# Optimization experiments

Hardware: AMD Instinct MI355X
Metric: run time of the kernel (lower is better)

The kernel has to match this reference:

```python
import jax, jax.numpy as jnp
import numpy as np


def setup_inputs() -> dict:
    key = jax.random.key(0)
    k1, k2 = jax.random.split(key)
    x = jax.random.normal(k1, (64, 64, 64, 64), dtype=jnp.float32)
    embeddings = jax.random.normal(k2, (400, 64), dtype=jnp.float32) * 0.1
    return {"x": x, "embeddings": embeddings}


def reference(x, embeddings):
    D = embeddings.shape[1]
    flat_x = x.reshape(-1, D)  # [N, D]
    # squared L2 distance via sum-of-squares + matmul: [N, K]
    distances = (
        jnp.sum(flat_x * flat_x, axis=1, keepdims=True)
        + jnp.sum(embeddings * embeddings, axis=1)
        - 2.0 * jnp.matmul(flat_x, embeddings.T)
    )
    encoding_indices = jnp.argmin(distances, axis=1)  # [N]
    quantized = jnp.take(embeddings, encoding_indices, axis=0)  # [N, D]
    return quantized.reshape(x.shape)
```

## Files before the change

kernel.cpp:

```cpp
#include <hip/hip_runtime.h>
#include <hip/hip_bf16.h>

#define D 64
#define K 400
#define KT 25
#define BLOCK 512
#define WPB (BLOCK / 64)
#define MA 4

typedef _Float16 f16x8 __attribute__((ext_vector_type(8)));
typedef float f32x4 __attribute__((ext_vector_type(4)));

__global__ __launch_bounds__(BLOCK, 1) void vq_mfma(
    const float* __restrict__ x,
    const float* __restrict__ emb,
    float* __restrict__ out,
    int nrows) {
  __shared__ __align__(16) _Float16 sB[KT][4][64][8];
  __shared__ float s_nnorm[K];

  const int tid = threadIdx.x;

  for (int e = tid; e < KT * 4 * 64; e += BLOCK) {
    int t = e >> 8;
    int f = (e >> 6) & 3;
    int l = e & 63;
    int code = t * 16 + (l & 15);
    int kb = ((l >> 4) << 3) + ((f >> 1) << 5);
    const float* ep = emb + code * D + kb;
    float v[8];
    *(float4*)&v[0] = *(const float4*)ep;
    *(float4*)&v[4] = *(const float4*)(ep + 4);
    _Float16 h[8];
    if ((f & 1) == 0) {
#pragma unroll
      for (int j = 0; j < 8; ++j) h[j] = (_Float16)(2.0f * v[j]);
    } else {
#pragma unroll
      for (int j = 0; j < 8; ++j) {
        float s = 2.0f * v[j];
        _Float16 hh = (_Float16)s;
        float r = s - (float)hh;
        h[j] = (_Float16)(r * 2048.0f);
      }
    }
    *(f16x8*)&sB[t][f][l][0] = *(f16x8*)&h[0];
  }
  for (int k = tid; k < K; k += BLOCK) {
    const float* ep = emb + k * D;
    float s = 0.f;
#pragma unroll
    for (int d = 0; d < D; ++d) s = fmaf(ep[d], ep[d], s);
    s_nnorm[k] = -s;
  }
  __syncthreads();

  const int lane = tid & 63;
  const int wid = tid >> 6;
  const int gw = blockIdx.x * WPB + wid;
  const int nw = gridDim.x * WPB;
  const int l15 = lane & 15;
  const int q = lane >> 4;

  const f32x4 zero4 = {0.f, 0.f, 0.f, 0.f};

  const int ngrp = nrows >> 6;
  for (int p = gw; p < ngrp; p += nw) {
    const int row0 = p << 6;

    f16x8 xh[MA][2], xl[MA][2];
#pragma unroll
    for (int a = 0; a < MA; ++a)
#pragma unroll
      for (int c = 0; c < 2; ++c) {
        const float* xp =
            x + (size_t)(row0 + a * 16 + l15) * D + q * 8 + c * 32;
        float v[8];
        *(float4*)&v[0] = *(const float4*)xp;
        *(float4*)&v[4] = *(const float4*)(xp + 4);
        _Float16 hh[8], ll[8];
#pragma unroll
        for (int j = 0; j < 8; ++j) {
          _Float16 h = (_Float16)v[j];
          float r = v[j] - (float)h;
          hh[j] = h;
          ll[j] = (_Float16)(r * 2048.0f);
        }
        xh[a][c] = *(f16x8*)&hh[0];
        xl[a][c] = *(f16x8*)&ll[0];
      }

    float bestm[MA][4];
    int bestt[MA][4];
#pragma unroll
    for (int a = 0; a < MA; ++a)
#pragma unroll
      for (int i = 0; i < 4; ++i) {
        bestm[a][i] = -3.4e38f;
        bestt[a][i] = 0;
      }

    f16x8 bh0 = *(const f16x8*)&sB[0][0][lane][0];
    f16x8 bl0 = *(const f16x8*)&sB[0][1][lane][0];
    f16x8 bh1 = *(const f16x8*)&sB[0][2][lane][0];
    f16x8 bl1 = *(const f16x8*)&sB[0][3][lane][0];
    float nn = s_nnorm[l15];

    for (int t = 0; t < KT; ++t) {
      int tn = (t + 1 < KT) ? t + 1 : 0;
      f16x8 nbh0 = *(const f16x8*)&sB[tn][0][lane][0];
      f16x8 nbl0 = *(const f16x8*)&sB[tn][1][lane][0];
      f16x8 nbh1 = *(const f16x8*)&sB[tn][2][lane][0];
      f16x8 nbl1 = *(const f16x8*)&sB[tn][3][lane][0];
      float nnn = s_nnorm[tn * 16 + l15];

      f32x4 nrm4 = {nn, nn, nn, nn};
#pragma unroll
      for (int a = 0; a < MA; ++a) {
        f32x4 ah, al;
        ah = __builtin_amdgcn_mfma_f32_16x16x32_f16(xh[a][0], bh0, nrm4, 0, 0, 0);
        ah = __builtin_amdgcn_mfma_f32_16x16x32_f16(xh[a][1], bh1, ah, 0, 0, 0);
        al = __builtin_amdgcn_mfma_f32_16x16x32_f16(xh[a][0], bl0, zero4, 0, 0, 0);
        al = __builtin_amdgcn_mfma_f32_16x16x32_f16(xl[a][0], bh0, al, 0, 0, 0);
        al = __builtin_amdgcn_mfma_f32_16x16x32_f16(xh[a][1], bl1, al, 0, 0, 0);
        al = __builtin_amdgcn_mfma_f32_16x16x32_f16(xl[a][1], bh1, al, 0, 0, 0);
#pragma unroll
        for (int i = 0; i < 4; ++i) {
          float m = fmaf(al[i], 4.8828125e-4f, ah[i]);
          bool gt = m > bestm[a][i];
          bestm[a][i] = gt ? m : bestm[a][i];
          bestt[a][i] = gt ? t : bestt[a][i];
        }
      }
      bh0 = nbh0; bl0 = nbl0; bh1 = nbh1; bl1 = nbl1; nn = nnn;
    }

#pragma unroll
    for (int a = 0; a < MA; ++a) {
      float bv[4];
      int bk[4];
#pragma unroll
      for (int i = 0; i < 4; ++i) {
        bv[i] = bestm[a][i];
        bk[i] = bestt[a][i] * 16 + l15;
      }
#pragma unroll
      for (int m = 1; m <= 8; m <<= 1) {
#pragma unroll
        for (int i = 0; i < 4; ++i) {
          float ov = __shfl_xor(bv[i], m, 64);
          int ok = __shfl_xor(bk[i], m, 64);
          bool take = (ov > bv[i]) || ((ov == bv[i]) && (ok < bk[i]));
          bv[i] = take ? ov : bv[i];
          bk[i] = take ? ok : bk[i];
        }
      }
      int j = (lane >> 2) & 3;
      int k01 = (j & 1) ? bk[1] : bk[0];
      int k23 = (j & 1) ? bk[3] : bk[2];
      int kk = (j & 2) ? k23 : k01;
      int r = row0 + a * 16 + (lane >> 2);
      const float4* src = (const float4*)(emb + kk * D + (lane & 3) * 16);
      float4* dst = (float4*)(out + (size_t)r * D + (lane & 3) * 16);
#pragma unroll
      for (int s = 0; s < 4; ++s) dst[s] = src[s];
    }
  }
}

extern "C" void kernel_launch(void* const* d_in, const int* in_sizes, int n_in,
                              void* d_out, int out_size, void* d_ws, size_t ws_size,
                              hipStream_t stream) {
  const float* x = (const float*)d_in[0];
  const float* emb = (const float*)d_in[1];
  float* out = (float*)d_out;
  int nrows = in_sizes[0] / D;
  vq_mfma<<<256, BLOCK, 0, stream>>>(x, emb, out, nrows);
}
```

Before: 151.1 us.

## Precompute codebook fragments in a prep kernel and read them from global memory

Codebook fp16 hi/lo fragment conversion and norms move into a separate prep kernel that writes to workspace. The main kernel stops staging them in shared memory: each wave reads B fragments directly from global/L2 and handles one 64-row group. The launch changes from a persistent 256-block grid to one wave per row group with 4 waves per block, dropping per-block prep work and LDS usage to allow more occupancy. The cost is an extra kernel launch, repeated global loads of the codebook per wave, and a naive fallback kernel when the workspace is too small.

```diff
diff --git a/kernel.cpp b/kernel.cpp
--- a/kernel.cpp
+++ b/kernel.cpp
@@ -4,168 +4,203 @@
 #define D 64
 #define K 400
 #define KT 25
-#define BLOCK 512
-#define WPB (BLOCK / 64)
 #define MA 4
 
 typedef _Float16 f16x8 __attribute__((ext_vector_type(8)));
 typedef float f32x4 __attribute__((ext_vector_type(4)));
 
-__global__ __launch_bounds__(BLOCK, 1) void vq_mfma(
+#define WS_FRAG_HALVES (KT * 4 * 64 * 8)
+#define WS_NEED (WS_FRAG_HALVES * 2 + K * 4)
+
+__global__ __launch_bounds__(256) void vq_prep(const float* __restrict__ emb,
+                                               _Float16* __restrict__ wfrag,
+                                               float* __restrict__ wnnorm) {
+  const int t = blockIdx.x;
+  const int tid = threadIdx.x;
+  const int f = tid >> 6;
+  const int l = tid & 63;
+  const int code = t * 16 + (l & 15);
+  const int kb = ((l >> 4) << 3) + ((f >> 1) << 5);
+  const float* ep = emb + code * D + kb;
+  float v[8];
+  *(float4*)&v[0] = *(const float4*)ep;
+  *(float4*)&v[4] = *(const float4*)(ep + 4);
+  _Float16 h[8];
+  if ((f & 1) == 0) {
+#pragma unroll
+    for (int j = 0; j < 8; ++j) h[j] = (_Float16)(2.0f * v[j]);
+  } else {
+#pragma unroll
+    for (int j = 0; j < 8; ++j) {
+      float s = 2.0f * v[j];
+      _Float16 hh = (_Float16)s;
+      float r = s - (float)hh;
+      h[j] = (_Float16)(r * 2048.0f);
+    }
+  }
+  *(f16x8*)(wfrag + (size_t)((t * 4 + f) * 64 + l) * 8) = *(f16x8*)&h[0];
+  if (tid < 16) {
+    const float* np = emb + (t * 16 + tid) * D;
+    float s = 0.f;
+#pragma unroll
+    for (int d = 0; d < D; ++d) s = fmaf(np[d], np[d], s);
+    wnnorm[t * 16 + tid] = -s;
+  }
+}
+
+__global__ __launch_bounds__(256, 4) void vq_main(
     const float* __restrict__ x,
+    const _Float16* __restrict__ wfrag,
+    const float* __restrict__ wnnorm,
     const float* __restrict__ emb,
     float* __restrict__ out,
     int nrows) {
-  __shared__ __align__(16) _Float16 sB[KT][4][64][8];
-  __shared__ float s_nnorm[K];
-
-  const int tid = threadIdx.x;
-
-  for (int e = tid; e < KT * 4 * 64; e += BLOCK) {
-    int t = e >> 8;
-    int f = (e >> 6) & 3;
-    int l = e & 63;
-    int code = t * 16 + (l & 15);
-    int kb = ((l >> 4) << 3) + ((f >> 1) << 5);
-    const float* ep = emb + code * D + kb;
-    float v[8];
-    *(float4*)&v[0] = *(const float4*)ep;
-    *(float4*)&v[4] = *(const float4*)(ep + 4);
-    _Float16 h[8];
-    if ((f & 1) == 0) {
-#pragma unroll
-      for (int j = 0; j < 8; ++j) h[j] = (_Float16)(2.0f * v[j]);
-    } else {
-#pragma unroll
-      for (int j = 0; j < 8; ++j) {
-        float s = 2.0f * v[j];
-        _Float16 hh = (_Float16)s;
-        float r = s - (float)hh;
-        h[j] = (_Float16)(r * 2048.0f);
-      }
-    }
-    *(f16x8*)&sB[t][f][l][0] = *(f16x8*)&h[0];
-  }
-  for (int k = tid; k < K; k += BLOCK) {
-    const float* ep = emb + k * D;
-    float s = 0.f;
-#pragma unroll
-    for (int d = 0; d < D; ++d) s = fmaf(ep[d], ep[d], s);
-    s_nnorm[k] = -s;
-  }
-  __syncthreads();
-
-  const int lane = tid & 63;
-  const int wid = tid >> 6;
-  const int gw = blockIdx.x * WPB + wid;
-  const int nw = gridDim.x * WPB;
+  const int lane = threadIdx.x & 63;
+  const int wid = threadIdx.x >> 6;
+  const int gw = blockIdx.x * 4 + wid;
+  const int row0 = gw << 6;
+  if (row0 >= nrows) return;
+
   const int l15 = lane & 15;
   const int q = lane >> 4;
-
   const f32x4 zero4 = {0.f, 0.f, 0.f, 0.f};
-
-  const int ngrp = nrows >> 6;
-  for (int p = gw; p < ngrp; p += nw) {
-    const int row0 = p << 6;
-
-    f16x8 xh[MA][2], xl[MA][2];
-#pragma unroll
-    for (int a = 0; a < MA; ++a)
-#pragma unroll
-      for (int c = 0; c < 2; ++c) {
-        const float* xp =
-            x + (size_t)(row0 + a * 16 + l15) * D + q * 8 + c * 32;
-        float v[8];
-        *(float4*)&v[0] = *(const float4*)xp;
-        *(float4*)&v[4] = *(const float4*)(xp + 4);
-        _Float16 hh[8], ll[8];
-#pragma unroll
-        for (int j = 0; j < 8; ++j) {
-          _Float16 h = (_Float16)v[j];
-          float r = v[j] - (float)h;
-          hh[j] = h;
-          ll[j] = (_Float16)(r * 2048.0f);
-        }
-        xh[a][c] = *(f16x8*)&hh[0];
-        xl[a][c] = *(f16x8*)&ll[0];
+  const f16x8* B = (const f16x8*)wfrag;
+
+  f16x8 xh[MA][2], xl[MA][2];
+#pragma unroll
+  for (int a = 0; a < MA; ++a)
+#pragma unroll
+    for (int c = 0; c < 2; ++c) {
+      const float* xp = x + (size_t)(row0 + a * 16 + l15) * D + q * 8 + c * 32;
+      float v[8];
+      *(float4*)&v[0] = *(const float4*)xp;
+      *(float4*)&v[4] = *(const float4*)(xp + 4);
+      _Float16 hh[8], ll[8];
+#pragma unroll
+      for (int j = 0; j < 8; ++j) {
+        _Float16 h = (_Float16)v[j];
+        float r = v[j] - (float)h;
+        hh[j] = h;
+        ll[j] = (_Float16)(r * 2048.0f);
       }
-
-    float bestm[MA][4];
-    int bestt[MA][4];
-#pragma unroll
-    for (int a = 0; a < MA; ++a)
+      xh[a][c] = *(f16x8*)&hh[0];
+      xl[a][c] = *(f16x8*)&ll[0];
+    }
+
+  float bestm[MA][4];
+  int bestt[MA][4];
+#pragma unroll
+  for (int a = 0; a < MA; ++a)
+#pragma unroll
+    for (int i = 0; i < 4; ++i) {
+      bestm[a][i] = -3.4e38f;
+      bestt[a][i] = 0;
+    }
+
+  f16x8 bh0 = B[0 * 64 + lane];
+  f16x8 bl0 = B[1 * 64 + lane];
+  f16x8 bh1 = B[2 * 64 + lane];
+  f16x8 bl1 = B[3 * 64 + lane];
+  float nn = wnnorm[l15];
+
+  for (int t = 0; t < KT; ++t) {
+    int tn = (t + 1 < KT) ? t + 1 : 0;
+    f16x8 nbh0 = B[(tn * 4 + 0) * 64 + lane];
+    f16x8 nbl0 = B[(tn * 4 + 1) * 64 + lane];
+    f16x8 nbh1 = B[(tn * 4 + 2) * 64 + lane];
+    f16x8 nbl1 = B[(tn * 4 + 3) * 64 + lane];
+    float nnn = wnnorm[tn * 16 + l15];
+
+    f32x4 nrm4 = {nn, nn, nn, nn};
+#pragma unroll
+    for (int a = 0; a < MA; ++a) {
+      f32x4 ah, al;
+      ah = __builtin_amdgcn_mfma_f32_16x16x32_f16(xh[a][0], bh0, nrm4, 0, 0, 0);
+      ah = __builtin_amdgcn_mfma_f32_16x16x32_f16(xh[a][1], bh1, ah, 0, 0, 0);
+      al = __builtin_amdgcn_mfma_f32_16x16x32_f16(xh[a][0], bl0, zero4, 0, 0, 0);
+      al = __builtin_amdgcn_mfma_f32_16x16x32_f16(xl[a][0], bh0, al, 0, 0, 0);
+      al = __builtin_amdgcn_mfma_f32_16x16x32_f16(xh[a][1], bl1, al, 0, 0, 0);
+      al = __builtin_amdgcn_mfma_f32_16x16x32_f16(xl[a][1], bh1, al, 0, 0, 0);
 #pragma unroll
       for (int i = 0; i < 4; ++i) {
-        bestm[a][i] = -3.4e38f;
-        bestt[a][i] = 0;
+        float m = fmaf(al[i], 4.8828125e-4f, ah[i]);
+        bool gt = m > bestm[a][i];
+        bestm[a][i] = gt ? m : bestm[a][i];
+        bestt[a][i] = gt ? t : bestt[a][i];
       }
-
-    f16x8 bh0 = *(const f16x8*)&sB[0][0][lane][0];
-    f16x8 bl0 = *(const f16x8*)&sB[0][1][lane][0];
-    f16x8 bh1 = *(const f16x8*)&sB[0][2][lane][0];
-    f16x8 bl1 = *(const f16x8*)&sB[0][3][lane][0];
-    float nn = s_nnorm[l15];
-
-    for (int t = 0; t < KT; ++t) {
-      int tn = (t + 1 < KT) ? t + 1 : 0;
-      f16x8 nbh0 = *(const f16x8*)&sB[tn][0][lane][0];
-      f16x8 nbl0 = *(const f16x8*)&sB[tn][1][lane][0];
-      f16x8 nbh1 = *(const f16x8*)&sB[tn][2][lane][0];
-      f16x8 nbl1 = *(const f16x8*)&sB[tn][3][lane][0];
-      float nnn = s_nnorm[tn * 16 + l15];
-
-      f32x4 nrm4 = {nn, nn, nn, nn};
-#pragma unroll
-      for (int a = 0; a < MA; ++a) {
-        f32x4 ah, al;
-        ah = __builtin_amdgcn_mfma_f32_16x16x32_f16(xh[a][0], bh0, nrm4, 0, 0, 0);
-        ah = __builtin_amdgcn_mfma_f32_16x16x32_f16(xh[a][1], bh1, ah, 0, 0, 0);
-        al = __builtin_amdgcn_mfma_f32_16x16x32_f16(xh[a][0], bl0, zero4, 0, 0, 0);
-        al = __builtin_amdgcn_mfma_f32_16x16x32_f16(xl[a][0], bh0, al, 0, 0, 0);
-        al = __builtin_amdgcn_mfma_f32_16x16x32_f16(xh[a][1], bl1, al, 0, 0, 0);
-        al = __builtin_amdgcn_mfma_f32_16x16x32_f16(xl[a][1], bh1, al, 0, 0, 0);
-#pragma unroll
-        for (int i = 0; i < 4; ++i) {
-          float m = fmaf(al[i], 4.8828125e-4f, ah[i]);
-          bool gt = m > bestm[a][i];
-          bestm[a][i] = gt ? m : bestm[a][i];
-          bestt[a][i] = gt ? t : bestt[a][i];
-        }
+    }
+    bh0 = nbh0; bl0 = nbl0; bh1 = nbh1; bl1 = nbl1; nn = nnn;
+  }
+
+#pragma unroll
+  for (int a = 0; a < MA; ++a) {
+    float bv[4];
+    int bk[4];
+#pragma unroll
+    for (int i = 0; i < 4; ++i) {
+      bv[i] = bestm[a][i];
+      bk[i] = bestt[a][i] * 16 + l15;
+    }
+#pragma unroll
+    for (int m = 1; m <= 8; m <<= 1) {
+#pragma unroll
+      for (int i = 0; i < 4; ++i) {
+        float ov = __shfl_xor(bv[i], m, 64);
+        int ok = __shfl_xor(bk[i], m, 64);
+        bool take = (ov > bv[i]) || ((ov == bv[i]) && (ok < bk[i]));
+        bv[i] = take ? ov : bv[i];
+        bk[i] = take ? ok : bk[i];
       }
-      bh0 = nbh0; bl0 = nbl0; bh1 = nbh1; bl1 = nbl1; nn = nnn;
-    }
-
-#pragma unroll
-    for (int a = 0; a < MA; ++a) {
-      float bv[4];
-      int bk[4];
-#pragma unroll
-      for (int i = 0; i < 4; ++i) {
-        bv[i] = bestm[a][i];
-        bk[i] = bestt[a][i] * 16 + l15;
-      }
-#pragma unroll
-      for (int m = 1; m <= 8; m <<= 1) {
-#pragma unroll
-        for (int i = 0; i < 4; ++i) {
-          float ov = __shfl_xor(bv[i], m, 64);
-          int ok = __shfl_xor(bk[i], m, 64);
-          bool take = (ov > bv[i]) || ((ov == bv[i]) && (ok < bk[i]));
-          bv[i] = take ? ov : bv[i];
-          bk[i] = take ? ok : bk[i];
-        }
-      }
-      int j = (lane >> 2) & 3;
-      int k01 = (j & 1) ? bk[1] : bk[0];
-      int k23 = (j & 1) ? bk[3] : bk[2];
-      int kk = (j & 2) ? k23 : k01;
-      int r = row0 + a * 16 + (lane >> 2);
-      const float4* src = (const float4*)(emb + kk * D + (lane & 3) * 16);
-      float4* dst = (float4*)(out + (size_t)r * D + (lane & 3) * 16);
-#pragma unroll
-      for (int s = 0; s < 4; ++s) dst[s] = src[s];
-    }
-  }
+    }
+    int j = (lane >> 2) & 3;
+    int k01 = (j & 1) ? bk[1] : bk[0];
+    int k23 = (j & 1) ? bk[3] : bk[2];
+    int kk = (j & 2) ? k23 : k01;
+    int r = row0 + a * 16 + (lane >> 2);
+    const float4* src = (const float4*)(emb + kk * D + (lane & 3) * 16);
+    float4* dst = (float4*)(out + (size_t)r * D + (lane & 3) * 16);
+#pragma unroll
+    for (int s = 0; s < 4; ++s) dst[s] = src[s];
+  }
+}
+
+__global__ __launch_bounds__(256) void vq_naive(const float* __restrict__ x,
+                                                const float* __restrict__ emb,
+                                                float* __restrict__ out,
+                                                int nrows) {
+  __shared__ float s_norm[K];
+  for (int k = threadIdx.x; k < K; k += blockDim.x) {
+    const float* e = emb + k * D;
+    float s = 0.f;
+#pragma unroll
+    for (int d = 0; d < D; ++d) s = fmaf(e[d], e[d], s);
+    s_norm[k] = s;
+  }
+  __syncthreads();
+  int r = blockIdx.x * blockDim.x + threadIdx.x;
+  if (r >= nrows) return;
+  float xr[D];
+  const float4* xv = (const float4*)(x + (size_t)r * D);
+#pragma unroll
+  for (int j = 0; j < D / 4; ++j) {
+    float4 t = xv[j];
+    xr[4 * j] = t.x; xr[4 * j + 1] = t.y; xr[4 * j + 2] = t.z; xr[4 * j + 3] = t.w;
+  }
+  float best = 3.4e38f;
+  int bestk = 0;
+#pragma unroll 2
+  for (int k = 0; k < K; ++k) {
+    const float* e = emb + k * D;
+    float acc = 0.f;
+#pragma unroll
+    for (int d = 0; d < D; ++d) acc = fmaf(e[d], xr[d], acc);
+    float score = fmaf(-2.f, acc, s_norm[k]);
+    if (score < best) { best = score; bestk = k; }
+  }
+  float4* ov = (float4*)(out + (size_t)r * D);
+  const float4* ev = (const float4*)(emb + (size_t)bestk * D);
+#pragma unroll
+  for (int j = 0; j < D / 4; ++j) ov[j] = ev[j];
 }
 
 extern "C" void kernel_launch(void* const* d_in, const int* in_sizes, int n_in,
@@ -175,5 +210,17 @@
   const float* emb = (const float*)d_in[1];
   float* out = (float*)d_out;
   int nrows = in_sizes[0] / D;
-  vq_mfma<<<256, BLOCK, 0, stream>>>(x, emb, out, nrows);
-}
+
+  if (ws_size < (size_t)WS_NEED) {
+    vq_naive<<<(nrows + 255) / 256, 256, 0, stream>>>(x, emb, out, nrows);
+    return;
+  }
+
+  _Float16* wfrag = (_Float16*)d_ws;
+  float* wnnorm = (float*)((char*)d_ws + WS_FRAG_HALVES * 2);
+
+  vq_prep<<<KT, 256, 0, stream>>>(emb, wfrag, wnnorm);
+  int nwave = (nrows + 63) / 64;
+  int nblk = (nwave + 3) / 4;
+  vq_main<<<nblk, 256, 0, stream>>>(x, wfrag, wnnorm, emb, out, nrows);
+}
```

After: 211.5 us. 1.4x slower.
